# Optimization experiments

Measured on AMD Instinct MI355X. Metric: run time of the kernel, lower is better.

Reference implementation:

```python
import jax, jax.numpy as jnp
import numpy as np

B, S, E, H, D = 4, 2048, 1024, 16, 64  # batch, seq, embed, heads, head_dim


def setup_inputs() -> dict:
    key = jax.random.key(0)
    k1, k2, k3 = jax.random.split(key, 3)
    x = jax.random.normal(k1, (B, S, E), dtype=jnp.float32)
    qkv_w = jax.random.normal(k2, (E, H, 3 * D), dtype=jnp.float32) * (1.0 / np.sqrt(E))
    qkv_b = jnp.zeros((H, 3 * D), dtype=jnp.float32)
    out_w = jax.random.normal(k3, (H, D, E), dtype=jnp.float32) * (1.0 / np.sqrt(H * D))
    out_b = jnp.zeros((E,), dtype=jnp.float32)
    return {"x": x, "qkv_w": qkv_w, "qkv_b": qkv_b, "out_w": out_w, "out_b": out_b}


def _large_negative_number(dtype):
    return jnp.asarray(-0.7 * jnp.finfo(dtype).max, dtype=dtype)


def reference(x, qkv_w, qkv_b, out_w, out_b):
    # qkv projection: LinearGeneral(E -> (H, 3D))
    qkv = jnp.einsum('bse,ehd->bshd', x, qkv_w) + qkv_b  # [B,S,H,3D]
    q, k, v = jnp.split(qkv, 3, axis=-1)  # each [B,S,H,D]
    logits = jnp.einsum('bqhd,bkhd->bhqk', q, k)  # [B,H,S,S]
    logits = logits / jnp.sqrt(jnp.asarray(q.shape[-1], logits.dtype))
    mask = jnp.tril(jnp.ones((q.shape[1], q.shape[1]), dtype=jnp.bool_))
    logits = jnp.where(mask, logits, _large_negative_number(logits.dtype))
    probs = jax.nn.softmax(logits, axis=-1)
    attn = jnp.einsum('bhqk,bkhd->bqhd', probs, v)  # [B,S,H,D]
    # output projection: LinearGeneral((H, D) -> E)
    return jnp.einsum('bqhd,hde->bqe', attn, out_w) + out_b
```

## Files before the change

### kernel.cpp

```cpp
#include <hip/hip_runtime.h>

typedef unsigned int u32;
typedef _Float16 f16;
typedef _Float16 f16x8 __attribute__((ext_vector_type(8)));
typedef _Float16 f16x4 __attribute__((ext_vector_type(4)));
typedef float f32x4 __attribute__((ext_vector_type(4)));

#define LOG2E 1.4426950408889634f

__device__ __forceinline__ void gl_lds16(const void* g, void* l) {
  __builtin_amdgcn_global_load_lds(
      (const __attribute__((address_space(1))) u32*)g,
      (__attribute__((address_space(3))) u32*)l, 16, 0, 0);
}

__device__ __forceinline__ f32x4 mfma16(f16x8 a, f16x8 b, f32x4 c) {
  return __builtin_amdgcn_mfma_f32_16x16x32_f16(a, b, c, 0, 0, 0);
}

__global__ void k_cvt(const float* __restrict__ in, f16* __restrict__ out, int n4) {
  int stride = gridDim.x * blockDim.x;
  for (int i = blockIdx.x * blockDim.x + threadIdx.x; i < n4; i += stride) {
    f32x4 v = *(const f32x4*)(in + (size_t)i * 4);
    f16x4 o;
    o[0] = (f16)v[0]; o[1] = (f16)v[1]; o[2] = (f16)v[2]; o[3] = (f16)v[3];
    *(f16x4*)(out + (size_t)i * 4) = o;
  }
}

__global__ void k_tconv(const float* __restrict__ in, f16* __restrict__ out, int R, int C) {
  __shared__ f16 tile[32][33];
  int c0 = blockIdx.x * 32, r0 = blockIdx.y * 32;
  int tx = threadIdx.x, ty = threadIdx.y;
#pragma unroll
  for (int i = ty; i < 32; i += 8)
    tile[i][tx] = (f16)in[(size_t)(r0 + i) * C + c0 + tx];
  __syncthreads();
#pragma unroll
  for (int i = ty; i < 32; i += 8)
    out[(size_t)(c0 + i) * R + r0 + tx] = tile[tx][i];
}

__global__ __launch_bounds__(256) void k_gemm_qkv(
    const f16* __restrict__ A, const f16* __restrict__ Bt,
    const float* __restrict__ bias,
    f16* __restrict__ qo, f16* __restrict__ ko2, f16* __restrict__ vto) {
  constexpr int K = 1024;
  __shared__ __align__(16) f16 As[128 * 32];
  __shared__ __align__(16) f16 Bs[128 * 32];
  const int bn = blockIdx.x * 128, bm = blockIdx.y * 128;
  const int t = threadIdx.x, lane = t & 63, w = t >> 6;
  const int wr = w >> 1, wc = w & 1;
  const int g = lane >> 4, rl = lane & 15;

  const int c0 = t, c1 = 256 + t;
  const int r0 = c0 >> 2, s0 = (c0 & 3) ^ ((r0 >> 1) & 3);
  const int r1 = c1 >> 2, s1 = (c1 & 3) ^ ((r1 >> 1) & 3);
  const f16* a0 = A + (size_t)(bm + r0) * K + s0 * 8;
  const f16* a1 = A + (size_t)(bm + r1) * K + s1 * 8;
  const f16* b0 = Bt + (size_t)(bn + r0) * K + s0 * 8;
  const f16* b1 = Bt + (size_t)(bn + r1) * K + s1 * 8;
  f16* lA0 = As + w * 512;
  f16* lA1 = As + 2048 + w * 512;
  f16* lB0 = Bs + w * 512;
  f16* lB1 = Bs + 2048 + w * 512;

  f32x4 acc[4][4] = {};

  for (int kt = 0; kt < K / 32; ++kt) {
    const int kof = kt * 32;
    gl_lds16(a0 + kof, lA0);
    gl_lds16(a1 + kof, lA1);
    gl_lds16(b0 + kof, lB0);
    gl_lds16(b1 + kof, lB1);
    __syncthreads();
    f16x8 af[4], bfr[4];
#pragma unroll
    for (int i = 0; i < 4; ++i) {
      int row = wr * 64 + i * 16 + rl;
      af[i] = *(const f16x8*)(As + row * 32 + ((g ^ ((row >> 1) & 3)) * 8));
      int col = wc * 64 + i * 16 + rl;
      bfr[i] = *(const f16x8*)(Bs + col * 32 + ((g ^ ((col >> 1) & 3)) * 8));
    }
#pragma unroll
    for (int i = 0; i < 4; ++i)
#pragma unroll
      for (int j = 0; j < 4; ++j)
        acc[i][j] = mfma16(af[i], bfr[j], acc[i][j]);
    __syncthreads();
  }

#pragma unroll
  for (int i = 0; i < 4; ++i)
#pragma unroll
    for (int j = 0; j < 4; ++j)
#pragma unroll
      for (int r = 0; r < 4; ++r) {
        int m = bm + wr * 64 + i * 16 + g * 4 + r;
        int n = bn + wc * 64 + j * 16 + rl;
        float v = acc[i][j][r] + bias[n];
        int b = m >> 11, s = m & 2047;
        int h = n / 192, rem = n - h * 192;
        int tsel = rem >> 6, d = rem & 63;
        size_t bh = (size_t)(b * 16 + h);
        if (tsel == 0)      qo[(bh * 2048 + s) * 64 + d] = (f16)(v * (0.125f * LOG2E));
        else if (tsel == 1) ko2[(bh * 2048 + s) * 64 + d] = (f16)v;
        else                vto[(bh * 64 + d) * 2048 + s] = (f16)v;
      }
}

__global__ __launch_bounds__(256, 4) void k_attn2(
    const f16* __restrict__ q, const f16* __restrict__ kgl,
    const f16* __restrict__ vt, f16* __restrict__ o) {
  constexpr int S = 2048;
  __shared__ __align__(16) f16 Ks[2][64 * 64];
  __shared__ __align__(16) f16 Vs[2][64 * 64];
  __shared__ __align__(16) f16 Ps[4][16 * 64];

  const int blk = blockIdx.x;
  const int sidx = blk >> 3;
  const int bh = (blk & 7) * 8 + (sidx & 7);
  const int qb = 15 - (sidx >> 3);

  const int t = threadIdx.x, lane = t & 63, w = t >> 6;
  const int g = lane >> 4, rl = lane & 15;

  const f16* qp = q + ((size_t)bh * S + qb * 128) * 64;
  const f16* kb = kgl + (size_t)bh * S * 64;
  const f16* vb = vt + (size_t)bh * 64 * S;

  f16x8 qf[2][2];
#pragma unroll
  for (int sub = 0; sub < 2; ++sub)
#pragma unroll
    for (int ks = 0; ks < 2; ++ks)
      qf[sub][ks] = *(const f16x8*)(qp + (size_t)(w * 32 + sub * 16 + rl) * 64 + ks * 32 + g * 8);

  f32x4 oacc[2][4] = {};
  float lrow[2] = {0.f, 0.f};

  const int srow = lane >> 3;
  const int sslot = (lane & 7) ^ srow;

  const int nkt = 2 * qb + 2;
  const int qmaxw = qb * 128 + w * 32 + 31;

  auto STAGE = [&](int bufi, int kt) {
#pragma unroll
    for (int i = 0; i < 2; ++i) {
      const int r0 = w * 16 + i * 8;
      gl_lds16(kb + (size_t)(kt * 64 + r0 + srow) * 64 + sslot * 8, &Ks[bufi][r0 * 64]);
      gl_lds16(vb + (size_t)(r0 + srow) * S + kt * 64 + sslot * 8, &Vs[bufi][r0 * 64]);
    }
  };

  STAGE(0, 0);
  __syncthreads();
  int buf = 0;

  for (int kt = 0; kt < nkt; ++kt) {
    if (kt + 1 < nkt) STAGE(buf ^ 1, kt + 1);

    if (kt * 64 <= qmaxw) {
      const f16* Kb = &Ks[buf][0];
      const f16* Vb = &Vs[buf][0];
#pragma unroll
      for (int sub = 0; sub < 2; ++sub) {
        const int qsub = qb * 128 + w * 32 + sub * 16;
        if (kt * 64 > qsub + 15) continue;

        f32x4 sT[4] = {};
#pragma unroll
        for (int j = 0; j < 4; ++j)
#pragma unroll
          for (int ks = 0; ks < 2; ++ks) {
            int row = j * 16 + rl;
            f16x8 kf = *(const f16x8*)(Kb + row * 64 + (((ks * 4 + g) ^ (rl & 7)) * 8));
            sT[j] = mfma16(kf, qf[sub][ks], sT[j]);
          }

        if (kt * 64 + 63 > qsub) {
#pragma unroll
          for (int j = 0; j < 4; ++j)
#pragma unroll
            for (int r = 0; r < 4; ++r)
              if (kt * 64 + j * 16 + g * 4 + r > qsub + rl) sT[j][r] = -1e30f;
        }

        float ps = 0.f;
#pragma unroll
        for (int j = 0; j < 4; ++j) {
          f16x4 pb;
#pragma unroll
          for (int r = 0; r < 4; ++r) {
            float p = exp2f(sT[j][r]);
            ps += p;
            pb[r] = (f16)p;
          }
          *(f16x4*)(&Ps[w][0] + rl * 64 + (((j * 2 + (g >> 1)) ^ (rl & 7)) * 8) + (g & 1) * 4) = pb;
        }
        lrow[sub] += ps;

        asm volatile("s_waitcnt lgkmcnt(0)" ::: "memory");
        __builtin_amdgcn_sched_barrier(0);

        f16x8 pf[2];
#pragma unroll
        for (int ks = 0; ks < 2; ++ks)
          pf[ks] = *(const f16x8*)(&Ps[w][0] + rl * 64 + (((ks * 4 + g) ^ (rl & 7)) * 8));

#pragma unroll
        for (int dj = 0; dj < 4; ++dj)
#pragma unroll
          for (int ks = 0; ks < 2; ++ks) {
            int vrow = dj * 16 + rl;
            f16x8 vf = *(const f16x8*)(Vb + vrow * 64 + (((ks * 4 + g) ^ (rl & 7)) * 8));
            oacc[sub][dj] = mfma16(pf[ks], vf, oacc[sub][dj]);
          }
      }
    }
    __syncthreads();
    buf ^= 1;
  }

  float rinv[2];
#pragma unroll
  for (int sub = 0; sub < 2; ++sub) {
    float s_ = lrow[sub];
    s_ += __shfl_xor(s_, 16, 64);
    s_ += __shfl_xor(s_, 32, 64);
    rinv[sub] = 1.0f / s_;
  }

  const int h = bh & 15;
  const size_t rowb = (size_t)(bh >> 4) * 2048 + qb * 128 + w * 32;
#pragma unroll
  for (int sub = 0; sub < 2; ++sub)
#pragma unroll
    for (int r = 0; r < 4; ++r) {
      float ri = __shfl(rinv[sub], g * 4 + r, 64);
#pragma unroll
      for (int dj = 0; dj < 4; ++dj)
        o[(rowb + sub * 16 + g * 4 + r) * 1024 + h * 64 + dj * 16 + rl] =
            (f16)(oacc[sub][dj][r] * ri);
    }
}

__global__ __launch_bounds__(256) void k_gemm_out(
    const f16* __restrict__ A, const f16* __restrict__ Bt,
    const float* __restrict__ bias, float* __restrict__ out) {
  constexpr int K = 1024;
  __shared__ __align__(16) f16 As[128 * 32];
  __shared__ __align__(16) f16 Bs[128 * 32];
  const int bn = blockIdx.x * 128, bm = blockIdx.y * 128;
  const int t = threadIdx.x, lane = t & 63, w = t >> 6;
  const int wr = w >> 1, wc = w & 1;
  const int g = lane >> 4, rl = lane & 15;

  const int c0 = t, c1 = 256 + t;
  const int r0 = c0 >> 2, s0 = (c0 & 3) ^ ((r0 >> 1) & 3);
  const int r1 = c1 >> 2, s1 = (c1 & 3) ^ ((r1 >> 1) & 3);
  const f16* a0 = A + (size_t)(bm + r0) * K + s0 * 8;
  const f16* a1 = A + (size_t)(bm + r1) * K + s1 * 8;
  const f16* b0 = Bt + (size_t)(bn + r0) * K + s0 * 8;
  const f16* b1 = Bt + (size_t)(bn + r1) * K + s1 * 8;
  f16* lA0 = As + w * 512;
  f16* lA1 = As + 2048 + w * 512;
  f16* lB0 = Bs + w * 512;
  f16* lB1 = Bs + 2048 + w * 512;

  f32x4 acc[4][4] = {};

  for (int kt = 0; kt < K / 32; ++kt) {
    const int kof = kt * 32;
    gl_lds16(a0 + kof, lA0);
    gl_lds16(a1 + kof, lA1);
    gl_lds16(b0 + kof, lB0);
    gl_lds16(b1 + kof, lB1);
    __syncthreads();
    f16x8 af[4], bfr[4];
#pragma unroll
    for (int i = 0; i < 4; ++i) {
      int row = wr * 64 + i * 16 + rl;
      af[i] = *(const f16x8*)(As + row * 32 + ((g ^ ((row >> 1) & 3)) * 8));
      int col = wc * 64 + i * 16 + rl;
      bfr[i] = *(const f16x8*)(Bs + col * 32 + ((g ^ ((col >> 1) & 3)) * 8));
    }
#pragma unroll
    for (int i = 0; i < 4; ++i)
#pragma unroll
      for (int j = 0; j < 4; ++j)
        acc[i][j] = mfma16(af[i], bfr[j], acc[i][j]);
    __syncthreads();
  }

#pragma unroll
  for (int i = 0; i < 4; ++i)
#pragma unroll
    for (int j = 0; j < 4; ++j)
#pragma unroll
      for (int r = 0; r < 4; ++r) {
        int m = bm + wr * 64 + i * 16 + g * 4 + r;
        int n = bn + wc * 64 + j * 16 + rl;
        out[(size_t)m * 1024 + n] = acc[i][j][r] + bias[n];
      }
}

extern "C" void kernel_launch(void* const* d_in, const int* in_sizes, int n_in,
                              void* d_out, int out_size, void* d_ws, size_t ws_size,
                              hipStream_t stream) {
  (void)in_sizes; (void)n_in; (void)out_size; (void)ws_size;
  const float* x    = (const float*)d_in[0];
  const float* wqkv = (const float*)d_in[1];
  const float* bqkv = (const float*)d_in[2];
  const float* wo   = (const float*)d_in[3];
  const float* bo   = (const float*)d_in[4];
  float* out = (float*)d_out;
  char* ws = (char*)d_ws;

  f16* xb    = (f16*)(ws + 0);
  f16* wqkvt = (f16*)(ws + 16777216);
  f16* wot   = (f16*)(ws + 23068672);
  f16* qws   = (f16*)(ws + 25165824);
  f16* kws   = (f16*)(ws + 41943040);
  f16* vtws  = (f16*)(ws + 58720256);
  f16* attnb = xb;

  k_cvt<<<2048, 256, 0, stream>>>(x, xb, 8388608 / 4);
  k_tconv<<<dim3(96, 32), dim3(32, 8), 0, stream>>>(wqkv, wqkvt, 1024, 3072);
  k_tconv<<<dim3(32, 32), dim3(32, 8), 0, stream>>>(wo, wot, 1024, 1024);
  k_gemm_qkv<<<dim3(24, 64), 256, 0, stream>>>(xb, wqkvt, bqkv, qws, kws, vtws);
  k_attn2<<<1024, 256, 0, stream>>>(qws, kws, vtws, attnb);
  k_gemm_out<<<dim3(8, 64), 256, 0, stream>>>(attnb, wot, bo, out);
}
```

Baseline: 197.8 us.

## Pipeline projection GEMMs with triple-buffered LDS and 128x256 tiles

```diff
diff --git a/kernel.cpp b/kernel.cpp
--- a/kernel.cpp
+++ b/kernel.cpp
@@ -41,53 +41,78 @@
     out[(size_t)(c0 + i) * R + r0 + tx] = tile[tx][i];
 }
 
-__global__ __launch_bounds__(256) void k_gemm_qkv(
+
+__global__ __launch_bounds__(512, 4) void k_gemm_qkv2(
     const f16* __restrict__ A, const f16* __restrict__ Bt,
     const float* __restrict__ bias,
     f16* __restrict__ qo, f16* __restrict__ ko2, f16* __restrict__ vto) {
-  constexpr int K = 1024;
-  __shared__ __align__(16) f16 As[128 * 32];
-  __shared__ __align__(16) f16 Bs[128 * 32];
-  const int bn = blockIdx.x * 128, bm = blockIdx.y * 128;
+  constexpr int NT = 32;
+  __shared__ __align__(16) f16 As[3 * 128 * 32];
+  __shared__ __align__(16) f16 Bs[3 * 256 * 32];
+  const int bn = blockIdx.x * 256, bm = blockIdx.y * 128;
   const int t = threadIdx.x, lane = t & 63, w = t >> 6;
-  const int wr = w >> 1, wc = w & 1;
+  const int wr = w >> 2, wc = w & 3;
   const int g = lane >> 4, rl = lane & 15;
-
-  const int c0 = t, c1 = 256 + t;
-  const int r0 = c0 >> 2, s0 = (c0 & 3) ^ ((r0 >> 1) & 3);
-  const int r1 = c1 >> 2, s1 = (c1 & 3) ^ ((r1 >> 1) & 3);
-  const f16* a0 = A + (size_t)(bm + r0) * K + s0 * 8;
-  const f16* a1 = A + (size_t)(bm + r1) * K + s1 * 8;
-  const f16* b0 = Bt + (size_t)(bn + r0) * K + s0 * 8;
-  const f16* b1 = Bt + (size_t)(bn + r1) * K + s1 * 8;
-  f16* lA0 = As + w * 512;
-  f16* lA1 = As + 2048 + w * 512;
-  f16* lB0 = Bs + w * 512;
-  f16* lB1 = Bs + 2048 + w * 512;
+  const int lr = lane >> 2, lp = lane & 3;
+
+  const int arow = w * 16 + lr;
+  const f16* aSrc = A + (size_t)(bm + arow) * 1024 + (lp ^ ((arow >> 1) & 3)) * 8;
+  const int brow0 = w * 32 + lr, brow1 = brow0 + 16;
+  const f16* bSrc0 = Bt + (size_t)(bn + brow0) * 1024 + (lp ^ ((brow0 >> 1) & 3)) * 8;
+  const f16* bSrc1 = Bt + (size_t)(bn + brow1) * 1024 + (lp ^ ((brow1 >> 1) & 3)) * 8;
+  f16* aDst = As + w * 512;
+  f16* bDst0 = Bs + w * 1024;
+  f16* bDst1 = bDst0 + 512;
 
   f32x4 acc[4][4] = {};
 
-  for (int kt = 0; kt < K / 32; ++kt) {
-    const int kof = kt * 32;
-    gl_lds16(a0 + kof, lA0);
-    gl_lds16(a1 + kof, lA1);
-    gl_lds16(b0 + kof, lB0);
-    gl_lds16(b1 + kof, lB1);
-    __syncthreads();
-    f16x8 af[4], bfr[4];
+  gl_lds16(aSrc, aDst);
+  gl_lds16(bSrc0, bDst0);
+  gl_lds16(bSrc1, bDst1);
+  gl_lds16(aSrc + 32, aDst + 4096);
+  gl_lds16(bSrc0 + 32, bDst0 + 8192);
+  gl_lds16(bSrc1 + 32, bDst1 + 8192);
+
+  int c = 0, cs = 2;
+#pragma unroll 1
+  for (int kt = 0; kt < NT; ++kt) {
+    if (kt + 1 < NT) { asm volatile("s_waitcnt vmcnt(3)" ::: "memory"); }
+    else             { asm volatile("s_waitcnt vmcnt(0)" ::: "memory"); }
+    __builtin_amdgcn_sched_barrier(0);
+    __builtin_amdgcn_s_barrier();
+    __builtin_amdgcn_sched_barrier(0);
+
+    if (kt + 2 < NT) {
+      const int ko = (kt + 2) * 32;
+      gl_lds16(aSrc + ko, aDst + cs * 4096);
+      gl_lds16(bSrc0 + ko, bDst0 + cs * 8192);
+      gl_lds16(bSrc1 + ko, bDst1 + cs * 8192);
+    }
+
+    const f16* Ab = As + c * 4096;
+    const f16* Bb = Bs + c * 8192;
+    f16x8 af[4], bf[4];
 #pragma unroll
     for (int i = 0; i < 4; ++i) {
-      int row = wr * 64 + i * 16 + rl;
-      af[i] = *(const f16x8*)(As + row * 32 + ((g ^ ((row >> 1) & 3)) * 8));
-      int col = wc * 64 + i * 16 + rl;
-      bfr[i] = *(const f16x8*)(Bs + col * 32 + ((g ^ ((col >> 1) & 3)) * 8));
-    }
+      const int r = wr * 64 + i * 16 + rl;
+      af[i] = *(const f16x8*)(Ab + r * 32 + ((g ^ ((r >> 1) & 3)) * 8));
+    }
+#pragma unroll
+    for (int j = 0; j < 4; ++j) {
+      const int rb = wc * 64 + j * 16 + rl;
+      bf[j] = *(const f16x8*)(Bb + rb * 32 + ((g ^ ((rb >> 1) & 3)) * 8));
+    }
+    __builtin_amdgcn_s_setprio(1);
 #pragma unroll
     for (int i = 0; i < 4; ++i)
 #pragma unroll
       for (int j = 0; j < 4; ++j)
-        acc[i][j] = mfma16(af[i], bfr[j], acc[i][j]);
-    __syncthreads();
+        acc[i][j] = mfma16(af[i], bf[j], acc[i][j]);
+    __builtin_amdgcn_s_setprio(0);
+    __builtin_amdgcn_sched_barrier(0);
+
+    c = (c == 2) ? 0 : c + 1;
+    cs = (cs == 2) ? 0 : cs + 1;
   }
 
 #pragma unroll
@@ -109,6 +134,90 @@
       }
 }
 
+__global__ __launch_bounds__(512, 4) void k_gemm_out2(
+    const f16* __restrict__ A, const f16* __restrict__ Bt,
+    const float* __restrict__ bias, float* __restrict__ out) {
+  constexpr int NT = 32;
+  __shared__ __align__(16) f16 As[3 * 128 * 32];
+  __shared__ __align__(16) f16 Bs[3 * 256 * 32];
+  const int bn = blockIdx.x * 256, bm = blockIdx.y * 128;
+  const int t = threadIdx.x, lane = t & 63, w = t >> 6;
+  const int wr = w >> 2, wc = w & 3;
+  const int g = lane >> 4, rl = lane & 15;
+  const int lr = lane >> 2, lp = lane & 3;
+
+  const int arow = w * 16 + lr;
+  const f16* aSrc = A + (size_t)(bm + arow) * 1024 + (lp ^ ((arow >> 1) & 3)) * 8;
+  const int brow0 = w * 32 + lr, brow1 = brow0 + 16;
+  const f16* bSrc0 = Bt + (size_t)(bn + brow0) * 1024 + (lp ^ ((brow0 >> 1) & 3)) * 8;
+  const f16* bSrc1 = Bt + (size_t)(bn + brow1) * 1024 + (lp ^ ((brow1 >> 1) & 3)) * 8;
+  f16* aDst = As + w * 512;
+  f16* bDst0 = Bs + w * 1024;
+  f16* bDst1 = bDst0 + 512;
+
+  f32x4 acc[4][4] = {};
+
+  gl_lds16(aSrc, aDst);
+  gl_lds16(bSrc0, bDst0);
+  gl_lds16(bSrc1, bDst1);
+  gl_lds16(aSrc + 32, aDst + 4096);
+  gl_lds16(bSrc0 + 32, bDst0 + 8192);
+  gl_lds16(bSrc1 + 32, bDst1 + 8192);
+
+  int c = 0, cs = 2;
+#pragma unroll 1
+  for (int kt = 0; kt < NT; ++kt) {
+    if (kt + 1 < NT) { asm volatile("s_waitcnt vmcnt(3)" ::: "memory"); }
+    else             { asm volatile("s_waitcnt vmcnt(0)" ::: "memory"); }
+    __builtin_amdgcn_sched_barrier(0);
+    __builtin_amdgcn_s_barrier();
+    __builtin_amdgcn_sched_barrier(0);
+
+    if (kt + 2 < NT) {
+      const int ko = (kt + 2) * 32;
+      gl_lds16(aSrc + ko, aDst + cs * 4096);
+      gl_lds16(bSrc0 + ko, bDst0 + cs * 8192);
+      gl_lds16(bSrc1 + ko, bDst1 + cs * 8192);
+    }
+
+    const f16* Ab = As + c * 4096;
+    const f16* Bb = Bs + c * 8192;
+    f16x8 af[4], bf[4];
+#pragma unroll
+    for (int i = 0; i < 4; ++i) {
+      const int r = wr * 64 + i * 16 + rl;
+      af[i] = *(const f16x8*)(Ab + r * 32 + ((g ^ ((r >> 1) & 3)) * 8));
+    }
+#pragma unroll
+    for (int j = 0; j < 4; ++j) {
+      const int rb = wc * 64 + j * 16 + rl;
+      bf[j] = *(const f16x8*)(Bb + rb * 32 + ((g ^ ((rb >> 1) & 3)) * 8));
+    }
+    __builtin_amdgcn_s_setprio(1);
+#pragma unroll
+    for (int i = 0; i < 4; ++i)
+#pragma unroll
+      for (int j = 0; j < 4; ++j)
+        acc[i][j] = mfma16(af[i], bf[j], acc[i][j]);
+    __builtin_amdgcn_s_setprio(0);
+    __builtin_amdgcn_sched_barrier(0);
+
+    c = (c == 2) ? 0 : c + 1;
+    cs = (cs == 2) ? 0 : cs + 1;
+  }
+
+#pragma unroll
+  for (int i = 0; i < 4; ++i)
+#pragma unroll
+    for (int j = 0; j < 4; ++j)
+#pragma unroll
+      for (int r = 0; r < 4; ++r) {
+        int m = bm + wr * 64 + i * 16 + g * 4 + r;
+        int n = bn + wc * 64 + j * 16 + rl;
+        out[(size_t)m * 1024 + n] = acc[i][j][r] + bias[n];
+      }
+}
+
 __global__ __launch_bounds__(256, 4) void k_attn2(
     const f16* __restrict__ q, const f16* __restrict__ kgl,
     const f16* __restrict__ vt, f16* __restrict__ o) {
@@ -244,66 +353,6 @@
         o[(rowb + sub * 16 + g * 4 + r) * 1024 + h * 64 + dj * 16 + rl] =
             (f16)(oacc[sub][dj][r] * ri);
     }
-}
-
-__global__ __launch_bounds__(256) void k_gemm_out(
-    const f16* __restrict__ A, const f16* __restrict__ Bt,
-    const float* __restrict__ bias, float* __restrict__ out) {
-  constexpr int K = 1024;
-  __shared__ __align__(16) f16 As[128 * 32];
-  __shared__ __align__(16) f16 Bs[128 * 32];
-  const int bn = blockIdx.x * 128, bm = blockIdx.y * 128;
-  const int t = threadIdx.x, lane = t & 63, w = t >> 6;
-  const int wr = w >> 1, wc = w & 1;
-  const int g = lane >> 4, rl = lane & 15;
-
-  const int c0 = t, c1 = 256 + t;
-  const int r0 = c0 >> 2, s0 = (c0 & 3) ^ ((r0 >> 1) & 3);
-  const int r1 = c1 >> 2, s1 = (c1 & 3) ^ ((r1 >> 1) & 3);
-  const f16* a0 = A + (size_t)(bm + r0) * K + s0 * 8;
-  const f16* a1 = A + (size_t)(bm + r1) * K + s1 * 8;
-  const f16* b0 = Bt + (size_t)(bn + r0) * K + s0 * 8;
-  const f16* b1 = Bt + (size_t)(bn + r1) * K + s1 * 8;
-  f16* lA0 = As + w * 512;
-  f16* lA1 = As + 2048 + w * 512;
-  f16* lB0 = Bs + w * 512;
-  f16* lB1 = Bs + 2048 + w * 512;
-
-  f32x4 acc[4][4] = {};
-
-  for (int kt = 0; kt < K / 32; ++kt) {
-    const int kof = kt * 32;
-    gl_lds16(a0 + kof, lA0);
-    gl_lds16(a1 + kof, lA1);
-    gl_lds16(b0 + kof, lB0);
-    gl_lds16(b1 + kof, lB1);
-    __syncthreads();
-    f16x8 af[4], bfr[4];
-#pragma unroll
-    for (int i = 0; i < 4; ++i) {
-      int row = wr * 64 + i * 16 + rl;
-      af[i] = *(const f16x8*)(As + row * 32 + ((g ^ ((row >> 1) & 3)) * 8));
-      int col = wc * 64 + i * 16 + rl;
-      bfr[i] = *(const f16x8*)(Bs + col * 32 + ((g ^ ((col >> 1) & 3)) * 8));
-    }
-#pragma unroll
-    for (int i = 0; i < 4; ++i)
-#pragma unroll
-      for (int j = 0; j < 4; ++j)
-        acc[i][j] = mfma16(af[i], bfr[j], acc[i][j]);
-    __syncthreads();
-  }
-
-#pragma unroll
-  for (int i = 0; i < 4; ++i)
-#pragma unroll
-    for (int j = 0; j < 4; ++j)
-#pragma unroll
-      for (int r = 0; r < 4; ++r) {
-        int m = bm + wr * 64 + i * 16 + g * 4 + r;
-        int n = bn + wc * 64 + j * 16 + rl;
-        out[(size_t)m * 1024 + n] = acc[i][j][r] + bias[n];
-      }
 }
 
 extern "C" void kernel_launch(void* const* d_in, const int* in_sizes, int n_in,
@@ -329,7 +378,7 @@
   k_cvt<<<2048, 256, 0, stream>>>(x, xb, 8388608 / 4);
   k_tconv<<<dim3(96, 32), dim3(32, 8), 0, stream>>>(wqkv, wqkvt, 1024, 3072);
   k_tconv<<<dim3(32, 32), dim3(32, 8), 0, stream>>>(wo, wot, 1024, 1024);
-  k_gemm_qkv<<<dim3(24, 64), 256, 0, stream>>>(xb, wqkvt, bqkv, qws, kws, vtws);
+  k_gemm_qkv2<<<dim3(12, 64), 512, 0, stream>>>(xb, wqkvt, bqkv, qws, kws, vtws);
   k_attn2<<<1024, 256, 0, stream>>>(qws, kws, vtws, attnb);
-  k_gemm_out<<<dim3(8, 64), 256, 0, stream>>>(attnb, wot, bo, out);
-}
+  k_gemm_out2<<<dim3(4, 64), 512, 0, stream>>>(attnb, wot, bo, out);
+}
```

Result: slower. 204.4 us (+3.3%).
